# Kernel tuning notes

Measured on AMD Instinct MI355X. Metric: run time of the kernel, lower is better.

## Reference

```python
import jax, jax.numpy as jnp
import numpy as np

EPS = 1e-8      # F.normalize eps in _cos_angle
TOPK = 4
DELTA = 1.0     # huber delta
EXTRA_FRAMES = (1, 3, 5, 7)            # teacher-only frames
SHARED = ((2, 1), (4, 2), (6, 3))      # (teacher_idx, student_idx) for shared frames


def _huber(e):
    ae = jnp.abs(e)
    return jnp.where(ae <= DELTA, 0.5 * e * e, DELTA * (ae - 0.5 * DELTA))


def _angles(R, H, Sh):
    # R: [b,r,d] ref, H: [b,r,k,d] sim_high, Sh: [b,s,d] shared.
    # Cosines of the three triplet angles computed via dot-product expansion,
    # avoiding any [b,r,s,k,d] intermediate. cos = (u.v)/(max(|u|,eps)*max(|v|,eps))
    RH  = jnp.einsum('brd,brkd->brk', R, H)
    RSh = jnp.einsum('brd,bsd->brs', R, Sh)
    HSh = jnp.einsum('brkd,bsd->brsk', H, Sh)
    Rn2  = jnp.sum(R * R, -1)        # [b,r]
    Hn2  = jnp.sum(H * H, -1)        # [b,r,k]
    Shn2 = jnp.sum(Sh * Sh, -1)      # [b,s]
    n_RSh = jnp.maximum(jnp.sqrt(jnp.maximum(Rn2[:, :, None] + Shn2[:, None, :] - 2 * RSh, 0.0)), EPS)          # |R-Sh| [b,r,s]
    n_RH  = jnp.maximum(jnp.sqrt(jnp.maximum(Rn2[:, :, None] + Hn2 - 2 * RH, 0.0)), EPS)                        # |R-H|  [b,r,k]
    n_HSh = jnp.maximum(jnp.sqrt(jnp.maximum(Hn2[:, :, None, :] + Shn2[:, None, :, None] - 2 * HSh, 0.0)), EPS) # |H-Sh| [b,r,s,k]
    # angle1: vertex=ref, u=Sh-R, v=H-R
    d1 = HSh - RSh[..., None] - RH[:, :, None, :] + Rn2[:, :, None, None]
    a1 = d1 / (n_RSh[..., None] * n_RH[:, :, None, :])
    # angle2: vertex=H, u=R-H, v=Sh-H
    d2 = RSh[..., None] - RH[:, :, None, :] - HSh + Hn2[:, :, None, :]
    a2 = d2 / (n_RH[:, :, None, :] * n_HSh)
    # angle3: vertex=Sh, u=R-Sh, v=H-Sh
    d3 = RH[:, :, None, :] - RSh[..., None] - HSh + Shn2[:, None, :, None]
    a3 = d3 / (n_RSh[..., None] * n_HSh)
    return a1, a2, a3


def setup_inputs() -> dict:
    key = jax.random.key(0)
    k1, k2, k3, k4 = jax.random.split(key, 4)
    B, S_T, P, D = 2, 8, 2048, 1024
    num_ref, num_shared = 128, 128
    teacher_feats = jax.random.normal(k1, (B, S_T, P, D), jnp.float32)
    student_feats = jax.random.normal(k2, (B, 4, P, D), jnp.float32)
    ref_perm = jax.random.permutation(k3, P)[:num_ref].astype(jnp.int32)
    shared_perm = jax.random.permutation(k4, P)[:num_shared].astype(jnp.int32)
    return {"teacher_feats": teacher_feats, "student_feats": student_feats,
            "ref_perm": ref_perm, "shared_perm": shared_perm}


def reference(teacher_feats, student_feats, ref_perm, shared_perm):
    tf = jax.lax.stop_gradient(teacher_feats)  # teacher is fully detached
    B, _, P, D = tf.shape
    num_ref = ref_perm.shape[0]
    num_shared = shared_perm.shape[0]
    ref_t = tf[:, 0, ref_perm, :]                 # [B,R,D]
    ref_s = student_feats[:, 0, ref_perm, :]
    # teacher-only frames, concatenated along patch dim -> [B, EP, D]
    extra = tf[:, jnp.array(EXTRA_FRAMES), :, :].reshape(B, -1, D)
    # cosine-similarity retrieval (selection_mode='topk')
    rtn = ref_t / jnp.maximum(jnp.linalg.norm(ref_t, axis=-1, keepdims=True), 1e-12)
    etn = extra / jnp.maximum(jnp.linalg.norm(extra, axis=-1, keepdims=True), 1e-12)
    sim = jnp.einsum('brd,bed->bre', rtn, etn)
    _, idx = jax.lax.top_k(sim, TOPK)             # [B,R,K]
    H = jnp.take_along_axis(extra, idx.reshape(B, -1, 1), axis=1).reshape(B, num_ref, TOPK, D)
    s1 = s2 = s3 = jnp.float32(0.0)
    for tidx, sidx in SHARED:
        Sh_t = tf[:, tidx, shared_perm, :]
        Sh_s = student_feats[:, sidx, shared_perm, :]
        a1t, a2t, a3t = _angles(ref_t, H, Sh_t)
        a1s, a2s, a3s = _angles(ref_s, H, Sh_s)
        s1 = s1 + _huber(a1s - a1t).sum()
        s2 = s2 + _huber(a2s - a2t).sum()
        s3 = s3 + _huber(a3s - a3t).sum()
    total = jnp.float32(len(SHARED) * B * num_ref * num_shared * TOPK)
    # angle weights all 1.0
    loss = s1 / total + s2 / total + s3 / total
    return loss
```

## Files before the change

### kernel.cpp

```cpp
#include <hip/hip_runtime.h>
#include <cstdint>
#include <cstddef>
#include <cfloat>
#include <climits>

#define D_DIM   1024
#define P_DIM   2048
#define NB      2
#define NR      128
#define NS      128
#define KTOP    4
#define E_DIM   8192
#define ANG_EPS 1e-8f
#define M_PAIR  768
#define N_PAIR  768

#define SIM_SLICES  4
#define SIM_KSLICE  256
#define SIM_STAGES  16
#define PAIR_SLICES 4
#define PAIR_KSLICE 256
#define PAIR_STAGES 16

__device__ __forceinline__ float dot4(float4 a, float4 b) {
  return a.x * b.x + a.y * b.y + a.z * b.z + a.w * b.w;
}

__device__ __forceinline__ float huber(float e) {
  float ae = fabsf(e);
  return ae <= 1.0f ? 0.5f * e * e : ae - 0.5f;
}

__device__ __forceinline__ bool better(float va, int ia, float vb, int ib) {
  return (va > vb) || (va == vb && ia < ib);
}

__device__ __forceinline__ float block_reduce_sum(float v, float* scratch) {
  #pragma unroll
  for (int o = 32; o > 0; o >>= 1) v += __shfl_down(v, o);
  __syncthreads();
  if ((threadIdx.x & 63) == 0) scratch[threadIdx.x >> 6] = v;
  __syncthreads();
  float r = 0.0f;
  int nw = (int)(blockDim.x >> 6);
  if ((int)threadIdx.x < nw) r = scratch[threadIdx.x];
  #pragma unroll
  for (int o = 2; o > 0; o >>= 1) r += __shfl_down(r, o);
  return r;
}

__global__ __launch_bounds__(256) void sim_gemm_kernel(const float* __restrict__ tf,
                                                       const int* __restrict__ ref_perm,
                                                       float* __restrict__ simP,
                                                       float* __restrict__ bn2P) {
  __shared__ float As[2][16][128];
  __shared__ float Bs[2][16][68];
  __shared__ const float* Arow[128];
  __shared__ const float* Brow[64];
  const int tid = threadIdx.x;
  const int b = blockIdx.z;
  const int slice = blockIdx.y;
  const int nbase = blockIdx.x * 64;
  const int kbase = slice * SIM_KSLICE;
  if (tid < 128) {
    Arow[tid] = tf + ((size_t)(b * 8) * P_DIM + ref_perm[tid]) * D_DIM + kbase;
  } else if (tid < 192) {
    int n = nbase + (tid - 128);
    Brow[tid - 128] = tf + ((size_t)(b * 8 + 1 + 2 * (n >> 11)) * P_DIM + (n & (P_DIM - 1))) * D_DIM + kbase;
  }
  __syncthreads();
  const int rowA = tid & 127;
  const int h8   = (tid >> 7) * 8;
  const int rowB = tid >> 2;
  const int lfB  = (tid & 3) * 4;
  const float* ap = Arow[rowA] + h8;
  const float* bp = Brow[rowB] + lfB;
  float4 a0 = *(const float4*)(ap);
  float4 a1 = *(const float4*)(ap + 4);
  float4 b0 = *(const float4*)(bp);
  float bn2 = dot4(b0, b0);

#define STASH(BUF) do { \
    As[BUF][h8 + 0][rowA] = a0.x; As[BUF][h8 + 1][rowA] = a0.y; \
    As[BUF][h8 + 2][rowA] = a0.z; As[BUF][h8 + 3][rowA] = a0.w; \
    As[BUF][h8 + 4][rowA] = a1.x; As[BUF][h8 + 5][rowA] = a1.y; \
    As[BUF][h8 + 6][rowA] = a1.z; As[BUF][h8 + 7][rowA] = a1.w; \
    Bs[BUF][lfB + 0][rowB] = b0.x; Bs[BUF][lfB + 1][rowB] = b0.y; \
    Bs[BUF][lfB + 2][rowB] = b0.z; Bs[BUF][lfB + 3][rowB] = b0.w; \
  } while (0)

  STASH(0);
  __syncthreads();

  const int tm8 = (tid >> 4) * 8;
  const int tn4 = (tid & 15) * 4;
  float acc[8][4] = {};
  for (int s = 0; s < SIM_STAGES; ++s) {
    const int cur = s & 1;
    const bool more = (s + 1 < SIM_STAGES);
    if (more) {
      ap += 16; bp += 16;
      a0 = *(const float4*)(ap);
      a1 = *(const float4*)(ap + 4);
      b0 = *(const float4*)(bp);
      bn2 += dot4(b0, b0);
    }
    #pragma unroll
    for (int kk = 0; kk < 16; ++kk) {
      float4 x0 = *(const float4*)&As[cur][kk][tm8];
      float4 x1 = *(const float4*)&As[cur][kk][tm8 + 4];
      float4 y0 = *(const float4*)&Bs[cur][kk][tn4];
      float av[8] = {x0.x, x0.y, x0.z, x0.w, x1.x, x1.y, x1.z, x1.w};
      float bv[4] = {y0.x, y0.y, y0.z, y0.w};
      #pragma unroll
      for (int i = 0; i < 8; ++i)
        #pragma unroll
        for (int j = 0; j < 4; ++j)
          acc[i][j] = fmaf(av[i], bv[j], acc[i][j]);
    }
    if (more) STASH(cur ^ 1);
    __syncthreads();
  }

  bn2 += __shfl_xor(bn2, 1);
  bn2 += __shfl_xor(bn2, 2);
  if ((tid & 3) == 0)
    bn2P[((size_t)slice * NB + b) * E_DIM + nbase + rowB] = bn2;

  float* base = simP + (((size_t)slice * NB + b) * NR) * E_DIM + nbase;
  #pragma unroll
  for (int i = 0; i < 8; ++i) {
    float4 o = make_float4(acc[i][0], acc[i][1], acc[i][2], acc[i][3]);
    *(float4*)(base + (size_t)(tm8 + i) * E_DIM + tn4) = o;
  }
#undef STASH
}

__global__ __launch_bounds__(256) void topk_kernel(const float* __restrict__ simP,
                                                   const float* __restrict__ bn2P,
                                                   int* __restrict__ tki) {
  __shared__ float sv[1024];
  __shared__ int si[1024];
  const int br = blockIdx.x;
  const int b = br >> 7;
  const size_t ST = (size_t)NB * NR * E_DIM;
  const size_t SN = (size_t)NB * E_DIM;
  const float* p = simP + (size_t)br * E_DIM;
  const float* q = bn2P + (size_t)b * E_DIM;
  float tv[4] = {-FLT_MAX, -FLT_MAX, -FLT_MAX, -FLT_MAX};
  int ti[4] = {INT_MAX, INT_MAX, INT_MAX, INT_MAX};
  for (int e = threadIdx.x; e < E_DIM; e += 256) {
    float s0 = p[e] + p[e + ST] + p[e + 2 * ST] + p[e + 3 * ST];
    float nn = q[e] + q[e + SN] + q[e + 2 * SN] + q[e + 3 * SN];
    float x = s0 * (1.0f / fmaxf(sqrtf(nn), 1e-12f));
    if (better(x, e, tv[3], ti[3])) {
      tv[3] = x; ti[3] = e;
      #pragma unroll
      for (int k = 3; k > 0; --k) {
        if (better(tv[k], ti[k], tv[k - 1], ti[k - 1])) {
          float fv = tv[k]; tv[k] = tv[k - 1]; tv[k - 1] = fv;
          int fi2 = ti[k]; ti[k] = ti[k - 1]; ti[k - 1] = fi2;
        }
      }
    }
  }
  int t = threadIdx.x;
  #pragma unroll
  for (int k = 0; k < 4; ++k) { sv[t * 4 + k] = tv[k]; si[t * 4 + k] = ti[k]; }
  for (int stride = 128; stride > 0; stride >>= 1) {
    __syncthreads();
    if (t < stride) {
      float av[4], bv2[4]; int ai[4], bi2[4];
      #pragma unroll
      for (int k = 0; k < 4; ++k) {
        av[k] = sv[t * 4 + k];               ai[k] = si[t * 4 + k];
        bv2[k] = sv[(t + stride) * 4 + k];   bi2[k] = si[(t + stride) * 4 + k];
      }
      float ov[4]; int oi[4]; int pa = 0, pb = 0;
      #pragma unroll
      for (int k = 0; k < 4; ++k) {
        bool takeA = (pa < 4) && (pb >= 4 || better(av[pa], ai[pa], bv2[pb], bi2[pb]));
        if (takeA) { ov[k] = av[pa]; oi[k] = ai[pa]; ++pa; }
        else       { ov[k] = bv2[pb]; oi[k] = bi2[pb]; ++pb; }
      }
      #pragma unroll
      for (int k = 0; k < 4; ++k) { sv[t * 4 + k] = ov[k]; si[t * 4 + k] = oi[k]; }
    }
  }
  __syncthreads();
  if (t < 4) tki[br * 4 + t] = si[t];
}

__global__ __launch_bounds__(256) void tables_kernel(const float* __restrict__ tf,
                                                     const float* __restrict__ sf,
                                                     const int* __restrict__ ref_perm,
                                                     const int* __restrict__ tki,
                                                     float* __restrict__ rt_n2, float* __restrict__ rs_n2,
                                                     float* __restrict__ hn2,
                                                     float* __restrict__ rh_t, float* __restrict__ rh_s) {
  __shared__ float scr[4];
  int br = blockIdx.x;
  int b = br >> 7, r = br & 127;
  const float* rt = tf + ((size_t)(b * 8) * P_DIM + ref_perm[r]) * D_DIM;
  const float* rs = sf + ((size_t)(b * 4) * P_DIM + ref_perm[r]) * D_DIM;
  int j = threadIdx.x * 4;
  float4 vt = *(const float4*)(rt + j);
  float4 vs = *(const float4*)(rs + j);
  float red;
  red = block_reduce_sum(dot4(vt, vt), scr); if (threadIdx.x == 0) rt_n2[br] = red;
  red = block_reduce_sum(dot4(vs, vs), scr); if (threadIdx.x == 0) rs_n2[br] = red;
  for (int k = 0; k < KTOP; ++k) {
    int e = tki[br * KTOP + k];
    const float* hp = tf + ((size_t)(b * 8 + 1 + 2 * (e >> 11)) * P_DIM + (e & (P_DIM - 1))) * D_DIM;
    float4 vh = *(const float4*)(hp + j);
    red = block_reduce_sum(dot4(vh, vh), scr); if (threadIdx.x == 0) hn2[br * KTOP + k] = red;
    red = block_reduce_sum(dot4(vt, vh), scr); if (threadIdx.x == 0) rh_t[br * KTOP + k] = red;
    red = block_reduce_sum(dot4(vs, vh), scr); if (threadIdx.x == 0) rh_s[br * KTOP + k] = red;
  }
}

__global__ __launch_bounds__(256) void sh_norms_kernel(const float* __restrict__ tf,
                                                       const float* __restrict__ sf,
                                                       const int* __restrict__ shared_perm,
                                                       float* __restrict__ shn2_t,
                                                       float* __restrict__ shn2_s) {
  __shared__ float scr[4];
  int row = blockIdx.x;
  int s = row & 127;
  int side = (row >> 7) & 1;
  int b = (row >> 8) & 1;
  int p = row >> 9;
  const float* ptr = (side == 0)
      ? tf + ((size_t)(b * 8 + 2 * p + 2) * P_DIM + shared_perm[s]) * D_DIM
      : sf + ((size_t)(b * 4 + p + 1) * P_DIM + shared_perm[s]) * D_DIM;
  float4 v = *(const float4*)(ptr + threadIdx.x * 4);
  float red = block_reduce_sum(dot4(v, v), scr);
  if (threadIdx.x == 0) {
    float* dst = (side == 0) ? shn2_t : shn2_s;
    dst[(p * 2 + b) * NS + s] = red;
  }
}

__global__ __launch_bounds__(256) void pair_gemm_kernel(const float* __restrict__ tf,
                                                        const float* __restrict__ sf,
                                                        const int* __restrict__ ref_perm,
                                                        const int* __restrict__ shared_perm,
                                                        const int* __restrict__ tki,
                                                        float* __restrict__ CpP) {
  __shared__ float As[2][16][128];
  __shared__ float Bs[2][16][68];
  __shared__ const float* Arow[128];
  __shared__ const float* Brow[64];
  const int tid = threadIdx.x;
  const int b = blockIdx.z & 1;
  const int slice = blockIdx.z >> 1;
  const int mbase = blockIdx.y * 128;
  const int nbase = blockIdx.x * 64;
  const int kbase = slice * PAIR_KSLICE;
  if (tid < 128) {
    int m = mbase + tid;
    const float* p;
    if (m < 128) {
      p = tf + ((size_t)(b * 8) * P_DIM + ref_perm[m]) * D_DIM;
    } else if (m < 256) {
      p = sf + ((size_t)(b * 4) * P_DIM + ref_perm[m - 128]) * D_DIM;
    } else {
      int h = m - 256, r = h >> 2, k = h & 3;
      int e = tki[(b * NR + r) * KTOP + k];
      p = tf + ((size_t)(b * 8 + 1 + 2 * (e >> 11)) * P_DIM + (e & (P_DIM - 1))) * D_DIM;
    }
    Arow[tid] = p + kbase;
  } else if (tid < 192) {
    int n = nbase + (tid - 128);
    int pr = n >> 8, rem = n & 255, side = rem >> 7, s = rem & 127;
    const float* p;
    if (side == 0) p = tf + ((size_t)(b * 8 + 2 * pr + 2) * P_DIM + shared_perm[s]) * D_DIM;
    else           p = sf + ((size_t)(b * 4 + pr + 1) * P_DIM + shared_perm[s]) * D_DIM;
    Brow[tid - 128] = p + kbase;
  }
  __syncthreads();
  const int rowA = tid & 127;
  const int h8   = (tid >> 7) * 8;
  const int rowB = tid >> 2;
  const int lfB  = (tid & 3) * 4;
  const float* ap = Arow[rowA] + h8;
  const float* bp = Brow[rowB] + lfB;
  float4 a0 = *(const float4*)(ap);
  float4 a1 = *(const float4*)(ap + 4);
  float4 b0 = *(const float4*)(bp);

#define STASH(BUF) do { \
    As[BUF][h8 + 0][rowA] = a0.x; As[BUF][h8 + 1][rowA] = a0.y; \
    As[BUF][h8 + 2][rowA] = a0.z; As[BUF][h8 + 3][rowA] = a0.w; \
    As[BUF][h8 + 4][rowA] = a1.x; As[BUF][h8 + 5][rowA] = a1.y; \
    As[BUF][h8 + 6][rowA] = a1.z; As[BUF][h8 + 7][rowA] = a1.w; \
    Bs[BUF][lfB + 0][rowB] = b0.x; Bs[BUF][lfB + 1][rowB] = b0.y; \
    Bs[BUF][lfB + 2][rowB] = b0.z; Bs[BUF][lfB + 3][rowB] = b0.w; \
  } while (0)

  STASH(0);
  __syncthreads();

  const int tm8 = (tid >> 4) * 8;
  const int tn4 = (tid & 15) * 4;
  float acc[8][4] = {};
  for (int s = 0; s < PAIR_STAGES; ++s) {
    const int cur = s & 1;
    const bool more = (s + 1 < PAIR_STAGES);
    if (more) {
      ap += 16; bp += 16;
      a0 = *(const float4*)(ap);
      a1 = *(const float4*)(ap + 4);
      b0 = *(const float4*)(bp);
    }
    #pragma unroll
    for (int kk = 0; kk < 16; ++kk) {
      float4 x0 = *(const float4*)&As[cur][kk][tm8];
      float4 x1 = *(const float4*)&As[cur][kk][tm8 + 4];
      float4 y0 = *(const float4*)&Bs[cur][kk][tn4];
      float av[8] = {x0.x, x0.y, x0.z, x0.w, x1.x, x1.y, x1.z, x1.w};
      float bv[4] = {y0.x, y0.y, y0.z, y0.w};
      #pragma unroll
      for (int i = 0; i < 8; ++i)
        #pragma unroll
        for (int j = 0; j < 4; ++j)
          acc[i][j] = fmaf(av[i], bv[j], acc[i][j]);
    }
    if (more) STASH(cur ^ 1);
    __syncthreads();
  }

  float* base = CpP + (((size_t)slice * NB + b) * M_PAIR + mbase) * N_PAIR + nbase;
  #pragma unroll
  for (int i = 0; i < 8; ++i) {
    float4 o = make_float4(acc[i][0], acc[i][1], acc[i][2], acc[i][3]);
    *(float4*)(base + (size_t)(tm8 + i) * N_PAIR + tn4) = o;
  }
#undef STASH
}

__global__ __launch_bounds__(128) void loss_kernel(const float* __restrict__ CpP,
                                                   const float* __restrict__ rt_n2,
                                                   const float* __restrict__ rs_n2,
                                                   const float* __restrict__ hn2,
                                                   const float* __restrict__ rh_t,
                                                   const float* __restrict__ rh_s,
                                                   const float* __restrict__ shn2_t,
                                                   const float* __restrict__ shn2_s,
                                                   float* __restrict__ acc) {
  __shared__ float scr[2];
  int r = blockIdx.x, b = blockIdx.y, p = blockIdx.z;
  int s = threadIdx.x;
  int br = b * NR + r;
  const size_t SLC = (size_t)NB * M_PAIR * N_PAIR;
  const float* Cb = CpP + (size_t)b * M_PAIR * N_PAIR;
  auto sumC = [&](int m, int n) -> float {
    const float* q = Cb + (size_t)m * N_PAIR + n;
    float v = 0.0f;
    #pragma unroll
    for (int sl = 0; sl < PAIR_SLICES; ++sl) v += q[sl * SLC];
    return v;
  };
  float Rt2 = rt_n2[br], Rs2 = rs_n2[br];
  float St2 = shn2_t[(p * 2 + b) * NS + s];
  float Ss2 = shn2_s[(p * 2 + b) * NS + s];
  float RSt = sumC(r, p * 256 + s);
  float RSs = sumC(128 + r, p * 256 + 128 + s);
  float sum = 0.0f;
  #pragma unroll
  for (int k = 0; k < KTOP; ++k) {
    float H2 = hn2[br * KTOP + k];
    float RHt = rh_t[br * KTOP + k];
    float RHs = rh_s[br * KTOP + k];
    float HSt = sumC(256 + r * 4 + k, p * 256 + s);
    float HSs = sumC(256 + r * 4 + k, p * 256 + 128 + s);
    float nRSt = fmaxf(sqrtf(fmaxf(Rt2 + St2 - 2.0f * RSt, 0.0f)), ANG_EPS);
    float nRHt = fmaxf(sqrtf(fmaxf(Rt2 + H2 - 2.0f * RHt, 0.0f)), ANG_EPS);
    float nHSt = fmaxf(sqrtf(fmaxf(H2 + St2 - 2.0f * HSt, 0.0f)), ANG_EPS);
    float a1t = (HSt - RSt - RHt + Rt2) / (nRSt * nRHt);
    float a2t = (RSt - RHt - HSt + H2) / (nRHt * nHSt);
    float a3t = (RHt - RSt - HSt + St2) / (nRSt * nHSt);
    float nRSs = fmaxf(sqrtf(fmaxf(Rs2 + Ss2 - 2.0f * RSs, 0.0f)), ANG_EPS);
    float nRHs = fmaxf(sqrtf(fmaxf(Rs2 + H2 - 2.0f * RHs, 0.0f)), ANG_EPS);
    float nHSs = fmaxf(sqrtf(fmaxf(H2 + Ss2 - 2.0f * HSs, 0.0f)), ANG_EPS);
    float a1s = (HSs - RSs - RHs + Rs2) / (nRSs * nRHs);
    float a2s = (RSs - RHs - HSs + H2) / (nRHs * nHSs);
    float a3s = (RHs - RSs - HSs + Ss2) / (nRSs * nHSs);
    sum += huber(a1s - a1t) + huber(a2s - a2t) + huber(a3s - a3t);
  }
  float tot = block_reduce_sum(sum, scr);
  if (threadIdx.x == 0) atomicAdd(acc, tot);
}

__global__ void finalize_kernel(const float* __restrict__ acc, float* __restrict__ out) {
  if (threadIdx.x == 0 && blockIdx.x == 0)
    out[0] = acc[0] * (1.0f / 393216.0f);
}

extern "C" void kernel_launch(void* const* d_in, const int* in_sizes, int n_in,
                              void* d_out, int out_size, void* d_ws, size_t ws_size,
                              hipStream_t stream) {
  const float* tf = (const float*)d_in[0];
  const float* sf = (const float*)d_in[1];
  const int* ref_perm = (const int*)d_in[2];
  const int* shared_perm = (const int*)d_in[3];
  float* ws = (float*)d_ws;

  float* simP   = ws;
  float* bn2P   = simP + (size_t)SIM_SLICES * NB * NR * E_DIM;
  float* CpP    = bn2P + (size_t)SIM_SLICES * NB * E_DIM;
  float* rt_n2  = CpP  + (size_t)PAIR_SLICES * NB * M_PAIR * N_PAIR;
  float* rs_n2  = rt_n2  + NB * NR;
  float* hn2    = rs_n2  + NB * NR;
  float* rh_t   = hn2    + NB * NR * KTOP;
  float* rh_s   = rh_t   + NB * NR * KTOP;
  float* shn2_t = rh_s   + NB * NR * KTOP;
  float* shn2_s = shn2_t + 3 * NB * NS;
  float* acc    = shn2_s + 3 * NB * NS;
  int*   tki    = (int*)(acc + 4);
  float* out = (float*)d_out;

  hipMemsetAsync(acc, 0, sizeof(float), stream);
  sim_gemm_kernel<<<dim3(E_DIM / 64, SIM_SLICES, NB), 256, 0, stream>>>(tf, ref_perm, simP, bn2P);
  topk_kernel<<<NB * NR, 256, 0, stream>>>(simP, bn2P, tki);
  tables_kernel<<<NB * NR, 256, 0, stream>>>(tf, sf, ref_perm, tki, rt_n2, rs_n2, hn2, rh_t, rh_s);
  sh_norms_kernel<<<3 * NB * 2 * NS, 256, 0, stream>>>(tf, sf, shared_perm, shn2_t, shn2_s);
  pair_gemm_kernel<<<dim3(N_PAIR / 64, M_PAIR / 128, NB * PAIR_SLICES), 256, 0, stream>>>(tf, sf, ref_perm, shared_perm, tki, CpP);
  loss_kernel<<<dim3(NR, NB, 3), 128, 0, stream>>>(CpP, rt_n2, rs_n2, hn2, rh_t, rh_s, shn2_t, shn2_s, acc);
  finalize_kernel<<<1, 64, 0, stream>>>(acc, out);
}
```

Before: 342.1 us.

## Use bf16 MFMA for similarity GEMM with exact fp32 rescoring of top-k candidates

The retrieval similarity GEMM now rounds inputs to bf16 and runs on MFMA 16x16x32 instructions with a 128x128 tile, replacing the fp32 FMA loop. To keep the top-k selection exact, the top-k kernel stores approximate scores, keeps every candidate within a margin of the fourth-best score, recomputes those candidates' cosine similarity in fp32 from the original features, and reselects the top 4. This targets the ALU-bound fp32 GEMM cost. It adds a candidate rescoring pass, and if more than 128 candidates fall inside the margin, the extra ones are dropped.

```diff
diff --git a/kernel.cpp b/kernel.cpp
--- a/kernel.cpp
+++ b/kernel.cpp
@@ -17,11 +17,16 @@
 
 #define SIM_SLICES  4
 #define SIM_KSLICE  256
-#define SIM_STAGES  16
 #define PAIR_SLICES 4
 #define PAIR_KSLICE 256
 #define PAIR_STAGES 16
 
+#define TOPK_DELTA  1.0f
+#define MAXCAND     128
+
+typedef short short8 __attribute__((ext_vector_type(8)));
+typedef float f32x4 __attribute__((ext_vector_type(4)));
+
 __device__ __forceinline__ float dot4(float4 a, float4 b) {
   return a.x * b.x + a.y * b.y + a.z * b.z + a.w * b.w;
 }
@@ -33,6 +38,15 @@
 
 __device__ __forceinline__ bool better(float va, int ia, float vb, int ib) {
   return (va > vb) || (va == vb && ia < ib);
+}
+
+__device__ __forceinline__ unsigned int f2bf(float x) {
+  union { float f; unsigned int u; } v; v.f = x;
+  unsigned int r = v.u + 0x7fffu + ((v.u >> 16) & 1u);
+  return r >> 16;
+}
+__device__ __forceinline__ unsigned int pk2bf(float x, float y) {
+  return f2bf(x) | (f2bf(y) << 16);
 }
 
 __device__ __forceinline__ float block_reduce_sum(float v, float* scratch) {
@@ -53,128 +67,176 @@
                                                        const int* __restrict__ ref_perm,
                                                        float* __restrict__ simP,
                                                        float* __restrict__ bn2P) {
-  __shared__ float As[2][16][128];
-  __shared__ float Bs[2][16][68];
+  __shared__ unsigned int Ah[128 * 20];
+  __shared__ unsigned int Bh[128 * 20];
   __shared__ const float* Arow[128];
-  __shared__ const float* Brow[64];
+  __shared__ const float* Brow[128];
   const int tid = threadIdx.x;
   const int b = blockIdx.z;
   const int slice = blockIdx.y;
-  const int nbase = blockIdx.x * 64;
+  const int nbase = blockIdx.x * 128;
   const int kbase = slice * SIM_KSLICE;
   if (tid < 128) {
     Arow[tid] = tf + ((size_t)(b * 8) * P_DIM + ref_perm[tid]) * D_DIM + kbase;
-  } else if (tid < 192) {
+  } else {
     int n = nbase + (tid - 128);
     Brow[tid - 128] = tf + ((size_t)(b * 8 + 1 + 2 * (n >> 11)) * P_DIM + (n & (P_DIM - 1))) * D_DIM + kbase;
   }
   __syncthreads();
-  const int rowA = tid & 127;
-  const int h8   = (tid >> 7) * 8;
-  const int rowB = tid >> 2;
-  const int lfB  = (tid & 3) * 4;
-  const float* ap = Arow[rowA] + h8;
-  const float* bp = Brow[rowB] + lfB;
-  float4 a0 = *(const float4*)(ap);
-  float4 a1 = *(const float4*)(ap + 4);
-  float4 b0 = *(const float4*)(bp);
-  float bn2 = dot4(b0, b0);
-
-#define STASH(BUF) do { \
-    As[BUF][h8 + 0][rowA] = a0.x; As[BUF][h8 + 1][rowA] = a0.y; \
-    As[BUF][h8 + 2][rowA] = a0.z; As[BUF][h8 + 3][rowA] = a0.w; \
-    As[BUF][h8 + 4][rowA] = a1.x; As[BUF][h8 + 5][rowA] = a1.y; \
-    As[BUF][h8 + 6][rowA] = a1.z; As[BUF][h8 + 7][rowA] = a1.w; \
-    Bs[BUF][lfB + 0][rowB] = b0.x; Bs[BUF][lfB + 1][rowB] = b0.y; \
-    Bs[BUF][lfB + 2][rowB] = b0.z; Bs[BUF][lfB + 3][rowB] = b0.w; \
-  } while (0)
-
-  STASH(0);
-  __syncthreads();
-
-  const int tm8 = (tid >> 4) * 8;
-  const int tn4 = (tid & 15) * 4;
-  float acc[8][4] = {};
-  for (int s = 0; s < SIM_STAGES; ++s) {
-    const int cur = s & 1;
-    const bool more = (s + 1 < SIM_STAGES);
-    if (more) {
-      ap += 16; bp += 16;
-      a0 = *(const float4*)(ap);
-      a1 = *(const float4*)(ap + 4);
-      b0 = *(const float4*)(bp);
-      bn2 += dot4(b0, b0);
-    }
-    #pragma unroll
-    for (int kk = 0; kk < 16; ++kk) {
-      float4 x0 = *(const float4*)&As[cur][kk][tm8];
-      float4 x1 = *(const float4*)&As[cur][kk][tm8 + 4];
-      float4 y0 = *(const float4*)&Bs[cur][kk][tn4];
-      float av[8] = {x0.x, x0.y, x0.z, x0.w, x1.x, x1.y, x1.z, x1.w};
-      float bv[4] = {y0.x, y0.y, y0.z, y0.w};
-      #pragma unroll
-      for (int i = 0; i < 8; ++i)
-        #pragma unroll
-        for (int j = 0; j < 4; ++j)
-          acc[i][j] = fmaf(av[i], bv[j], acc[i][j]);
-    }
-    if (more) STASH(cur ^ 1);
+
+  const int srow = tid >> 1;
+  const int shalf = (tid & 1) * 16;
+  const float* asrc = Arow[srow] + shalf;
+  const float* bsrc = Brow[srow] + shalf;
+
+  float4 av[4], bv[4];
+  #pragma unroll
+  for (int i = 0; i < 4; ++i) {
+    av[i] = *(const float4*)(asrc + 4 * i);
+    bv[i] = *(const float4*)(bsrc + 4 * i);
+  }
+
+  const int wave = tid >> 6;
+  const int lane = tid & 63;
+  const int fr = lane & 15;
+  const int q16 = (lane >> 4) * 16;
+  const char* Ab = (const char*)Ah;
+  const char* Bb = (const char*)Bh;
+
+  f32x4 acc[2][8];
+  #pragma unroll
+  for (int mt = 0; mt < 2; ++mt)
+    #pragma unroll
+    for (int nt = 0; nt < 8; ++nt)
+      #pragma unroll
+      for (int r = 0; r < 4; ++r) acc[mt][nt][r] = 0.0f;
+
+  float bn2 = 0.0f;
+  unsigned int* adst = Ah + srow * 20 + (tid & 1) * 8;
+  unsigned int* bdst = Bh + srow * 20 + (tid & 1) * 8;
+
+  for (int ck = 0; ck < 8; ++ck) {
+    bn2 += dot4(bv[0], bv[0]) + dot4(bv[1], bv[1]) + dot4(bv[2], bv[2]) + dot4(bv[3], bv[3]);
+    unsigned int ua[8], ub[8];
+    #pragma unroll
+    for (int i = 0; i < 4; ++i) {
+      ua[2 * i]     = pk2bf(av[i].x, av[i].y);
+      ua[2 * i + 1] = pk2bf(av[i].z, av[i].w);
+      ub[2 * i]     = pk2bf(bv[i].x, bv[i].y);
+      ub[2 * i + 1] = pk2bf(bv[i].z, bv[i].w);
+    }
     __syncthreads();
+    *(uint4*)(adst)     = make_uint4(ua[0], ua[1], ua[2], ua[3]);
+    *(uint4*)(adst + 4) = make_uint4(ua[4], ua[5], ua[6], ua[7]);
+    *(uint4*)(bdst)     = make_uint4(ub[0], ub[1], ub[2], ub[3]);
+    *(uint4*)(bdst + 4) = make_uint4(ub[4], ub[5], ub[6], ub[7]);
+    __syncthreads();
+    if (ck < 7) {
+      const float* an = asrc + (ck + 1) * 32;
+      const float* bn = bsrc + (ck + 1) * 32;
+      #pragma unroll
+      for (int i = 0; i < 4; ++i) {
+        av[i] = *(const float4*)(an + 4 * i);
+        bv[i] = *(const float4*)(bn + 4 * i);
+      }
+    }
+    short8 afr[2], bfr[8];
+    #pragma unroll
+    for (int mt = 0; mt < 2; ++mt)
+      afr[mt] = *(const short8*)(Ab + (wave * 32 + mt * 16 + fr) * 80 + q16);
+    #pragma unroll
+    for (int nt = 0; nt < 8; ++nt)
+      bfr[nt] = *(const short8*)(Bb + (nt * 16 + fr) * 80 + q16);
+    #pragma unroll
+    for (int mt = 0; mt < 2; ++mt)
+      #pragma unroll
+      for (int nt = 0; nt < 8; ++nt)
+        acc[mt][nt] = __builtin_amdgcn_mfma_f32_16x16x32_bf16(afr[mt], bfr[nt], acc[mt][nt], 0, 0, 0);
   }
 
   bn2 += __shfl_xor(bn2, 1);
-  bn2 += __shfl_xor(bn2, 2);
-  if ((tid & 3) == 0)
-    bn2P[((size_t)slice * NB + b) * E_DIM + nbase + rowB] = bn2;
+  if ((tid & 1) == 0)
+    bn2P[((size_t)slice * NB + b) * E_DIM + nbase + srow] = bn2;
 
   float* base = simP + (((size_t)slice * NB + b) * NR) * E_DIM + nbase;
-  #pragma unroll
-  for (int i = 0; i < 8; ++i) {
-    float4 o = make_float4(acc[i][0], acc[i][1], acc[i][2], acc[i][3]);
-    *(float4*)(base + (size_t)(tm8 + i) * E_DIM + tn4) = o;
-  }
-#undef STASH
+  const int crow = (lane >> 4) * 4;
+  #pragma unroll
+  for (int mt = 0; mt < 2; ++mt) {
+    #pragma unroll
+    for (int nt = 0; nt < 8; ++nt) {
+      int col = nt * 16 + fr;
+      #pragma unroll
+      for (int r = 0; r < 4; ++r) {
+        int m = wave * 32 + mt * 16 + crow + r;
+        base[(size_t)m * E_DIM + col] = acc[mt][nt][r];
+      }
+    }
+  }
 }
 
 __global__ __launch_bounds__(256) void topk_kernel(const float* __restrict__ simP,
                                                    const float* __restrict__ bn2P,
+                                                   const float* __restrict__ tf,
+                                                   const int* __restrict__ ref_perm,
                                                    int* __restrict__ tki) {
+  __shared__ float scores[E_DIM];
   __shared__ float sv[1024];
   __shared__ int si[1024];
+  __shared__ float candVal[MAXCAND];
+  __shared__ int candIdx[MAXCAND];
+  __shared__ int cnt;
+  const int tid = threadIdx.x;
   const int br = blockIdx.x;
   const int b = br >> 7;
+  const int r = br & 127;
   const size_t ST = (size_t)NB * NR * E_DIM;
   const size_t SN = (size_t)NB * E_DIM;
   const float* p = simP + (size_t)br * E_DIM;
   const float* q = bn2P + (size_t)b * E_DIM;
+  if (tid == 0) cnt = 0;
+
   float tv[4] = {-FLT_MAX, -FLT_MAX, -FLT_MAX, -FLT_MAX};
   int ti[4] = {INT_MAX, INT_MAX, INT_MAX, INT_MAX};
-  for (int e = threadIdx.x; e < E_DIM; e += 256) {
-    float s0 = p[e] + p[e + ST] + p[e + 2 * ST] + p[e + 3 * ST];
-    float nn = q[e] + q[e + SN] + q[e + 2 * SN] + q[e + 3 * SN];
-    float x = s0 * (1.0f / fmaxf(sqrtf(nn), 1e-12f));
-    if (better(x, e, tv[3], ti[3])) {
-      tv[3] = x; ti[3] = e;
-      #pragma unroll
-      for (int k = 3; k > 0; --k) {
-        if (better(tv[k], ti[k], tv[k - 1], ti[k - 1])) {
-          float fv = tv[k]; tv[k] = tv[k - 1]; tv[k - 1] = fv;
-          int fi2 = ti[k]; ti[k] = ti[k - 1]; ti[k - 1] = fi2;
+  for (int e4 = tid * 4; e4 < E_DIM; e4 += 1024) {
+    float4 s = *(const float4*)(p + e4);
+    float4 s1 = *(const float4*)(p + ST + e4);
+    float4 s2 = *(const float4*)(p + 2 * ST + e4);
+    float4 s3 = *(const float4*)(p + 3 * ST + e4);
+    float4 n0 = *(const float4*)(q + e4);
+    float4 n1 = *(const float4*)(q + SN + e4);
+    float4 n2 = *(const float4*)(q + 2 * SN + e4);
+    float4 n3 = *(const float4*)(q + 3 * SN + e4);
+    float sj[4] = {s.x + s1.x + s2.x + s3.x, s.y + s1.y + s2.y + s3.y,
+                   s.z + s1.z + s2.z + s3.z, s.w + s1.w + s2.w + s3.w};
+    float nj[4] = {n0.x + n1.x + n2.x + n3.x, n0.y + n1.y + n2.y + n3.y,
+                   n0.z + n1.z + n2.z + n3.z, n0.w + n1.w + n2.w + n3.w};
+    #pragma unroll
+    for (int j = 0; j < 4; ++j) {
+      int e = e4 + j;
+      float x = sj[j] * rsqrtf(fmaxf(nj[j], 1e-24f));
+      scores[e] = x;
+      if (better(x, e, tv[3], ti[3])) {
+        tv[3] = x; ti[3] = e;
+        #pragma unroll
+        for (int k = 3; k > 0; --k) {
+          if (better(tv[k], ti[k], tv[k - 1], ti[k - 1])) {
+            float fv = tv[k]; tv[k] = tv[k - 1]; tv[k - 1] = fv;
+            int fi2 = ti[k]; ti[k] = ti[k - 1]; ti[k - 1] = fi2;
+          }
         }
       }
     }
   }
-  int t = threadIdx.x;
-  #pragma unroll
-  for (int k = 0; k < 4; ++k) { sv[t * 4 + k] = tv[k]; si[t * 4 + k] = ti[k]; }
+  #pragma unroll
+  for (int k = 0; k < 4; ++k) { sv[tid * 4 + k] = tv[k]; si[tid * 4 + k] = ti[k]; }
   for (int stride = 128; stride > 0; stride >>= 1) {
     __syncthreads();
-    if (t < stride) {
+    if (tid < stride) {
       float av[4], bv2[4]; int ai[4], bi2[4];
       #pragma unroll
       for (int k = 0; k < 4; ++k) {
-        av[k] = sv[t * 4 + k];               ai[k] = si[t * 4 + k];
-        bv2[k] = sv[(t + stride) * 4 + k];   bi2[k] = si[(t + stride) * 4 + k];
+        av[k] = sv[tid * 4 + k];               ai[k] = si[tid * 4 + k];
+        bv2[k] = sv[(tid + stride) * 4 + k];   bi2[k] = si[(tid + stride) * 4 + k];
       }
       float ov[4]; int oi[4]; int pa = 0, pb = 0;
       #pragma unroll
@@ -184,11 +246,63 @@
         else       { ov[k] = bv2[pb]; oi[k] = bi2[pb]; ++pb; }
       }
       #pragma unroll
-      for (int k = 0; k < 4; ++k) { sv[t * 4 + k] = ov[k]; si[t * 4 + k] = oi[k]; }
-    }
-  }
-  __syncthreads();
-  if (t < 4) tki[br * 4 + t] = si[t];
+      for (int k = 0; k < 4; ++k) { sv[tid * 4 + k] = ov[k]; si[tid * 4 + k] = oi[k]; }
+    }
+  }
+  __syncthreads();
+  const float tau = sv[3] - TOPK_DELTA;
+
+  for (int e4 = tid * 4; e4 < E_DIM; e4 += 1024) {
+    #pragma unroll
+    for (int j = 0; j < 4; ++j) {
+      int e = e4 + j;
+      if (scores[e] >= tau) {
+        int pos = atomicAdd(&cnt, 1);
+        if (pos < MAXCAND) candIdx[pos] = e;
+      }
+    }
+  }
+  __syncthreads();
+  int cntc = min(cnt, MAXCAND);
+
+  const float* R = tf + ((size_t)(b * 8) * P_DIM + ref_perm[r]) * D_DIM;
+  const int wave = tid >> 6;
+  const int lane = tid & 63;
+  for (int c = wave; c < cntc; c += 4) {
+    int e = candIdx[c];
+    const float* E = tf + ((size_t)(b * 8 + 1 + 2 * (e >> 11)) * P_DIM + (e & (P_DIM - 1))) * D_DIM;
+    float d = 0.0f, n2 = 0.0f;
+    #pragma unroll
+    for (int i = 0; i < 4; ++i) {
+      float4 rv = *(const float4*)(R + lane * 16 + i * 4);
+      float4 ev = *(const float4*)(E + lane * 16 + i * 4);
+      d += dot4(rv, ev);
+      n2 += dot4(ev, ev);
+    }
+    #pragma unroll
+    for (int o = 32; o > 0; o >>= 1) { d += __shfl_xor(d, o); n2 += __shfl_xor(n2, o); }
+    if (lane == 0) candVal[c] = d / fmaxf(sqrtf(n2), 1e-12f);
+  }
+  __syncthreads();
+  if (tid == 0) {
+    float bv[4] = {-FLT_MAX, -FLT_MAX, -FLT_MAX, -FLT_MAX};
+    int bi[4] = {INT_MAX, INT_MAX, INT_MAX, INT_MAX};
+    for (int c = 0; c < cntc; ++c) {
+      float x = candVal[c]; int e = candIdx[c];
+      if (better(x, e, bv[3], bi[3])) {
+        bv[3] = x; bi[3] = e;
+        #pragma unroll
+        for (int k = 3; k > 0; --k) {
+          if (better(bv[k], bi[k], bv[k - 1], bi[k - 1])) {
+            float fv = bv[k]; bv[k] = bv[k - 1]; bv[k - 1] = fv;
+            int fi2 = bi[k]; bi[k] = bi[k - 1]; bi[k - 1] = fi2;
+          }
+        }
+      }
+    }
+    #pragma unroll
+    for (int k = 0; k < 4; ++k) tki[br * 4 + k] = bi[k];
+  }
 }
 
 __global__ __launch_bounds__(256) void tables_kernel(const float* __restrict__ tf,
@@ -421,8 +535,8 @@
   float* out = (float*)d_out;
 
   hipMemsetAsync(acc, 0, sizeof(float), stream);
-  sim_gemm_kernel<<<dim3(E_DIM / 64, SIM_SLICES, NB), 256, 0, stream>>>(tf, ref_perm, simP, bn2P);
-  topk_kernel<<<NB * NR, 256, 0, stream>>>(simP, bn2P, tki);
+  sim_gemm_kernel<<<dim3(E_DIM / 128, SIM_SLICES, NB), 256, 0, stream>>>(tf, ref_perm, simP, bn2P);
+  topk_kernel<<<NB * NR, 256, 0, stream>>>(simP, bn2P, tf, ref_perm, tki);
   tables_kernel<<<NB * NR, 256, 0, stream>>>(tf, sf, ref_perm, tki, rt_n2, rs_n2, hn2, rh_t, rh_s);
   sh_norms_kernel<<<3 * NB * 2 * NS, 256, 0, stream>>>(tf, sf, shared_perm, shn2_t, shn2_s);
   pair_gemm_kernel<<<dim3(N_PAIR / 64, M_PAIR / 128, NB * PAIR_SLICES), 256, 0, stream>>>(tf, sf, ref_perm, shared_perm, tki, CpP);
```

Result: no change. 343.5 us (+0.4%).
